# Optimization experiments

Hardware: AMD Instinct MI355X
Metric: run time of the kernel (lower is better)

The kernel has to match this reference:

```python
import jax, jax.numpy as jnp
import numpy as np
import math

B, HR, WR, C = 8, 128, 128, 192
WS, SS = 8, 4
NH, SPH, CHH = 8, 6, 2
DH = C // NH  # 24
AREA = WS * WS
MID = max(C // 4, 8)
NWIN = (HR // WS) * (WR // WS)
LOGMAX = math.log(100.0)

def _rel_pos_index(ws):
    coords = np.stack(np.meshgrid(np.arange(ws), np.arange(ws), indexing='ij')).reshape(2, -1)
    rel = (coords[:, :, None] - coords[:, None, :]).transpose(1, 2, 0).copy()
    rel[:, :, 0] += ws - 1
    rel[:, :, 1] += ws - 1
    rel[:, :, 0] *= 2 * ws - 1
    return rel.sum(-1)  # (AREA, AREA)

def _attn_mask(H, W, ws, ss):
    img = np.zeros((H, W))
    sl = (slice(0, -ws), slice(-ws, -ss), slice(-ss, None))
    cnt = 0
    for hs in sl:
        for wsl in sl:
            img[hs, wsl] = cnt
            cnt += 1
    mw = img.reshape(H // ws, ws, W // ws, ws).transpose(0, 2, 1, 3).reshape(-1, ws * ws)
    am = mw[:, None, :] - mw[:, :, None]
    return np.where(am != 0, -100.0, 0.0).astype(np.float32)

REL_IDX = jnp.asarray(_rel_pos_index(WS))
ATTN_MASK = jnp.asarray(_attn_mask(HR, WR, WS, SS))  # (NWIN, AREA, AREA)

def _norm(v):
    return v / jnp.maximum(jnp.linalg.norm(v, axis=-1, keepdims=True), 1e-12)

def _ln(x, g, b):
    m = x.mean(-1, keepdims=True)
    v = x.var(-1, keepdims=True)
    return (x - m) / jnp.sqrt(v + 1e-5) * g + b

def _bn(x, g, b, m, v):
    return (x - m) / jnp.sqrt(v + 1e-5) * g + b

def _conv3(x, w):  # x: NHWC, w: (O,I,3,3) torch layout
    return jax.lax.conv_general_dilated(x, jnp.transpose(w, (2, 3, 1, 0)), (1, 1), 'SAME', dimension_numbers=('NHWC', 'HWIO', 'NHWC'))

def _forward(x, ln1_g, ln1_b, w_qkv, b_qkv, logit_sp, rpb_table, w_spp, b_spp, logit_ch, w_chp, b_chp, w_sp_proj, w_ch_proj, w_s2c1, w_s2c2, b_s2c2, w_c2s1, w_c2s2, b_c2s2, w_gs1, w_gs2, b_gs2, w_gc1, w_gc2, b_gc2, w_f1, bn1_g, bn1_b, bn1_m, bn1_v, w_f2, bn2_g, bn2_b, bn2_m, bn2_v, w_sg1, w_sg2, b_sg2, ln2_g, ln2_b, w_fc1, b_fc1, w_fc2, b_fc2):
    h = _ln(x, ln1_g, ln1_b)
    img = h.reshape(B, HR, WR, C)
    # qkv conv1x1; per-head channel blocks of 3*DH (faithful to torch view)
    qkv = (img @ w_qkv.T + b_qkv).reshape(B, HR, WR, NH, 3 * DH)
    # ---- spatial shifted-window cosine attention (heads 0:SPH) ----
    sp = jnp.roll(qkv[..., :SPH, :], (-SS, -SS), axis=(1, 2))
    nHw, nWw = HR // WS, WR // WS
    sp = sp.reshape(B, nHw, WS, nWw, WS, SPH, 3 * DH).transpose(0, 1, 3, 5, 2, 4, 6)
    sp = sp.reshape(B * NWIN, SPH, AREA, 3 * DH)
    q, k, v = jnp.split(sp, 3, axis=-1)
    attn = jnp.einsum('bhid,bhjd->bhij', _norm(q), _norm(k))
    attn = attn * jnp.exp(jnp.minimum(logit_sp, LOGMAX)).reshape(1, SPH, 1, 1)
    attn = attn + rpb_table[REL_IDX].transpose(2, 0, 1)[None]
    attn = attn.reshape(B, NWIN, SPH, AREA, AREA) + ATTN_MASK[None, :, None]
    attn = jax.nn.softmax(attn.reshape(B * NWIN, SPH, AREA, AREA), axis=-1)
    o = jnp.einsum('bhij,bhjd->bhid', attn, v)
    o = o.reshape(B, nHw, nWw, SPH, WS, WS, DH).transpose(0, 1, 4, 2, 5, 3, 6).reshape(B, HR, WR, SPH * DH)
    o = o @ w_spp.T + b_spp
    sp_out = jnp.roll(o, (SS, SS), axis=(1, 2)) @ w_sp_proj.T  # (B,H,W,C)
    # ---- channel cosine self-attention (heads SPH:NH) ----
    chq = qkv[..., SPH:, :].reshape(B, HR * WR, CHH, 3 * DH).transpose(0, 2, 3, 1)  # (B,hh,3dh,HW)
    qc, kc, vc = jnp.split(chq, 3, axis=2)
    a = jnp.einsum('bhci,bhdi->bhcd', _norm(qc), _norm(kc))
    a = jax.nn.softmax(a * jnp.exp(jnp.minimum(logit_ch, LOGMAX)).reshape(1, CHH, 1, 1), axis=-1)
    oc = jnp.einsum('bhcd,bhdi->bhci', a, vc).reshape(B, CHH * DH, HR * WR)
    oc = oc.transpose(0, 2, 1).reshape(B, HR, WR, CHH * DH)
    ch_out = (oc @ w_chp.T + b_chp) @ w_ch_proj.T  # (B,H,W,C)
    # ---- CFCA cross gating ----
    def mlp1(t, w1, w2, b2):
        return jax.nn.relu(t @ w1.T) @ w2.T + b2
    sp2ch = mlp1(sp_out, w_s2c1, w_s2c2, b_s2c2) * jax.nn.sigmoid(mlp1(sp_out.mean((1, 2), keepdims=True), w_gs1, w_gs2, b_gs2))
    ch2sp = mlp1(ch_out, w_c2s1, w_c2s2, b_c2s2) * jax.nn.sigmoid(mlp1(ch_out.mean((1, 2), keepdims=True), w_gc1, w_gc2, b_gc2))
    spf = sp_out + ch2sp
    chf = ch_out + sp2ch
    # ---- XFF fusion (BN in eval mode) ----
    f = jnp.concatenate([spf, chf], axis=-1) @ w_f1.T
    f = jax.nn.relu(_bn(f, bn1_g, bn1_b, bn1_m, bn1_v))
    f = jax.nn.relu(_bn(_conv3(f, w_f2), bn2_g, bn2_b, bn2_m, bn2_v))
    g = jax.nn.sigmoid(jax.nn.relu(_conv3(f, w_sg1)) @ w_sg2.T + b_sg2)
    fused = f * g + f
    # ---- transformer block residual + MLP ----
    x = x + fused.reshape(B, HR * WR, C)
    h2 = _ln(x, ln2_g, ln2_b)
    return x + (jax.nn.gelu(h2 @ w_fc1.T + b_fc1, approximate=False) @ w_fc2.T + b_fc2)

def setup_inputs() -> dict:
    keys = iter(jax.random.split(jax.random.key(0), 64))
    def rn(shape, s=0.02):
        return jax.random.normal(next(keys), shape, dtype=jnp.float32) * s
    z = lambda *s: jnp.zeros(s, dtype=jnp.float32)
    o = lambda *s: jnp.ones(s, dtype=jnp.float32)
    return {
        'x': jax.random.normal(next(keys), (B, HR * WR, C), dtype=jnp.float32),
        'ln1_g': o(C), 'ln1_b': z(C),
        'w_qkv': rn((3 * C, C)), 'b_qkv': z(3 * C),
        'logit_sp': jnp.full((SPH,), math.log(10.0), dtype=jnp.float32),
        'rpb_table': rn(((2 * WS - 1) ** 2, SPH)),
        'w_spp': rn((SPH * DH, SPH * DH)), 'b_spp': z(SPH * DH),
        'logit_ch': jnp.full((CHH,), math.log(10.0), dtype=jnp.float32),
        'w_chp': rn((CHH * DH, CHH * DH)), 'b_chp': z(CHH * DH),
        'w_sp_proj': rn((C, SPH * DH)), 'w_ch_proj': rn((C, CHH * DH)),
        'w_s2c1': rn((MID, C)), 'w_s2c2': rn((C, MID)), 'b_s2c2': z(C),
        'w_c2s1': rn((MID, C)), 'w_c2s2': rn((C, MID)), 'b_c2s2': z(C),
        'w_gs1': rn((MID, C)), 'w_gs2': rn((C, MID)), 'b_gs2': z(C),
        'w_gc1': rn((MID, C)), 'w_gc2': rn((C, MID)), 'b_gc2': z(C),
        'w_f1': rn((C, 2 * C)),
        'bn1_g': o(C), 'bn1_b': z(C), 'bn1_m': z(C), 'bn1_v': o(C),
        'w_f2': rn((C, C, 3, 3)),
        'bn2_g': o(C), 'bn2_b': z(C), 'bn2_m': z(C), 'bn2_v': o(C),
        'w_sg1': rn((C // 2, C, 3, 3)), 'w_sg2': rn((1, C // 2)), 'b_sg2': z(1),
        'ln2_g': o(C), 'ln2_b': z(C),
        'w_fc1': rn((4 * C, C)), 'b_fc1': z(4 * C), 'w_fc2': rn((C, 4 * C)), 'b_fc2': z(C),
    }

def reference(x, ln1_g, ln1_b, w_qkv, b_qkv, logit_sp, rpb_table, w_spp, b_spp, logit_ch, w_chp, b_chp, w_sp_proj, w_ch_proj, w_s2c1, w_s2c2, b_s2c2, w_c2s1, w_c2s2, b_c2s2, w_gs1, w_gs2, b_gs2, w_gc1, w_gc2, b_gc2, w_f1, bn1_g, bn1_b, bn1_m, bn1_v, w_f2, bn2_g, bn2_b, bn2_m, bn2_v, w_sg1, w_sg2, b_sg2, ln2_g, ln2_b, w_fc1, b_fc1, w_fc2, b_fc2):
    return _forward(x, ln1_g, ln1_b, w_qkv, b_qkv, logit_sp, rpb_table, w_spp, b_spp, logit_ch, w_chp, b_chp, w_sp_proj, w_ch_proj, w_s2c1, w_s2c2, b_s2c2, w_c2s1, w_c2s2, b_c2s2, w_gs1, w_gs2, b_gs2, w_gc1, w_gc2, b_gc2, w_f1, bn1_g, bn1_b, bn1_m, bn1_v, w_f2, bn2_g, bn2_b, bn2_m, bn2_v, w_sg1, w_sg2, b_sg2, ln2_g, ln2_b, w_fc1, b_fc1, w_fc2, b_fc2)
```

## Files before the change

### kernel.cpp

```cpp
#include <hip/hip_runtime.h>
#include <hip/hip_bf16.h>
#include <cstddef>

typedef __hip_bfloat16 bf16;
typedef unsigned short u16;
typedef unsigned int u32;
typedef short s16x8 __attribute__((ext_vector_type(8)));
typedef float f32x4 __attribute__((ext_vector_type(4)));

#define BATCH 8
#define HR 128
#define WR 128
#define CCH 192
#define HW (HR*WR)
#define MTOK (BATCH*HW)
#define SPH 6
#define SPC 432
#define CHC 144
#define NWIN 256
#define MIDC 48
#define PH 130
#define PHW (PH*PH)
#define LOGMAX 4.6051701859880914f

static const size_t OFF_A0    = 0;
static const size_t OFF_B0    = 113246208;
static const size_t OFF_C0    = 150994944;
static const size_t OFF_SMALL = 188743680;
static const size_t SO_STATS  = 0;
static const size_t SO_PGRAM  = 1048576;
static const size_t SO_PSS    = 1638400;
static const size_t SO_ATTNB  = 1687552;
static const size_t SO_MEANSP = 1724416;
static const size_t SO_MEANCH = 1732608;
static const size_t SO_GATES  = 1740800;
static const size_t SO_GATEC  = 1748992;
static const size_t SO_BCSP   = 1757184;
static const size_t SO_WCCH   = 1758208;
static const size_t SO_BCCH   = 1795072;
static const size_t SO_WFUSE  = 1796096;
static const size_t SO_WCSPB  = 1943552;
static const size_t SO_WQB    = 1998848;
static const size_t SO_WS2C1B = 2220032;
static const size_t SO_WC2S1B = 2238464;
static const size_t SO_WS2C2B = 2256896;
static const size_t SO_WC2S2B = 2275328;
static const size_t SO_WF1B   = 2293760;
static const size_t SO_WF2CB  = 2441216;
static const size_t SO_WSG1CB = 3104768;
static const size_t SO_WFC1B  = 3436544;
static const size_t SO_WFC2B  = 3731456;

__device__ __forceinline__ float b2f(bf16 x) { return __bfloat162float(x); }
__device__ __forceinline__ bf16  f2b(float x){ return __float2bfloat16(x); }
__device__ __forceinline__ u16   f2u(float x){
    bf16 h = __float2bfloat16(x);
    union { bf16 b; u16 u; } c; c.b = h; return c.u;
}
__device__ __forceinline__ float s2f(short s){
    union { u16 u; bf16 b; } c; c.u = (u16)s; return b2f(c.b);
}
__device__ __forceinline__ float u2f(u16 u){
    union { u16 u; bf16 b; } c; c.u = u; return b2f(c.b);
}
__device__ __forceinline__ int xcdswz(int b, int n){
    const int q = n >> 3, r = n & 7, x = b & 7, o = b >> 3;
    return (x < r) ? (x * (q + 1) + o) : (r * (q + 1) + (x - r) * q + o);
}

#define GBM 128
#define GBK 32
#define LDA 40

struct SegRaw { union { uint4 v; struct { float4 lo, hi; } f; } d; };

template<int AMODE, int EPI, int CBF, int BNT, int CPAD, int WPB>
__global__ __launch_bounds__(256)
void gemm_k(const void* __restrict__ A, const u16* __restrict__ W,
            const float* __restrict__ bias, void* __restrict__ Cv,
            int M, int N, int K,
            const float* __restrict__ stats, const float* __restrict__ lng,
            const float* __restrict__ lnb, const void* __restrict__ A2,
            const float* __restrict__ ep0, const float* __restrict__ ep1,
            const float* __restrict__ ep2, const float* __restrict__ ep3)
{
    constexpr int NF = BNT / 32;
    constexpr int NB = (BNT * 4 + 255) / 256;
    constexpr int ATILE = GBM * LDA;
    constexpr int BTILE = BNT * LDA;
    constexpr int BUFSZ = ATILE + BTILE;
    constexpr int CST   = BNT + 8;
    __shared__ u16 smem[2 * BUFSZ];

    const int tid  = threadIdx.x;
    const int lane = tid & 63;
    const int wid  = tid >> 6;
    const int wm   = (wid >> 1) * 64;
    const int wn   = (wid & 1) * (BNT / 2);
    const int m0   = xcdswz(blockIdx.y, gridDim.y) * GBM;
    const int n0   = blockIdx.x * BNT;
    const int row16 = lane & 15;
    const int hi    = lane >> 4;
    const int koff  = hi * 8;

    const int arow[2] = { tid >> 2, (tid + 256) >> 2 };
    const int akk     = (tid & 3) * 8;

    const u16* Wb = W;
    if constexpr (WPB) Wb = W + (size_t)(m0 >> 14) * 9216;

    float meanA[2], rstdA[2];
    if constexpr (AMODE == 1) {
        #pragma unroll
        for (int it = 0; it < 2; ++it) {
            const int m = m0 + arow[it];
            meanA[it] = stats[2*m]; rstdA[it] = stats[2*m+1];
        }
    }

    f32x4 acc[4][NF];
    #pragma unroll
    for (int mf = 0; mf < 4; ++mf)
        #pragma unroll
        for (int nf = 0; nf < NF; ++nf)
            acc[mf][nf] = (f32x4){0.f, 0.f, 0.f, 0.f};

    const int nsteps = (K + GBK - 1) / GBK;

    auto loadA = [&](int step, SegRaw seg[2]) {
        const int k0 = step * GBK;
        #pragma unroll
        for (int it = 0; it < 2; ++it) {
            const int m = m0 + arow[it];
            const int k = k0 + akk;
            SegRaw& s = seg[it];
            if (k >= K) { s.d.v = (uint4){0u,0u,0u,0u}; continue; }
            if constexpr (AMODE == 0) {
                s.d.v = *(const uint4*)((const u16*)A + (size_t)m * K + k);
            } else if constexpr (AMODE == 1) {
                const float* p = (const float*)A + (size_t)m * K + k;
                s.d.f.lo = *(const float4*)p; s.d.f.hi = *(const float4*)(p+4);
            } else if constexpr (AMODE == 2) {
                const u16* src = (k < CCH) ? (const u16*)A  + (size_t)m * CCH + k
                                           : (const u16*)A2 + (size_t)m * CCH + (k - CCH);
                s.d.v = *(const uint4*)src;
            } else if constexpr (AMODE == 3) {
                const int tap = k / CCH, c = k - tap * CCH;
                const int ky = tap / 3, kx = tap - ky * 3;
                const int b = m >> 14, pix = m & 16383;
                const int h = pix >> 7, w = pix & 127;
                s.d.v = *(const uint4*)((const u16*)A +
                        ((size_t)b * PHW + (size_t)(h + ky) * PH + (w + kx)) * CCH + c);
            } else {
                const int col = (k < 24) ? (48 + k) : (96 + k);
                s.d.v = *(const uint4*)((const u16*)A + (size_t)m * CHC + col);
            }
        }
    };
    auto loadB = [&](int step, SegRaw seg[NB]) {
        const int k0 = step * GBK;
        #pragma unroll
        for (int it = 0; it < NB; ++it) {
            const int s = tid + it * 256;
            const int n = n0 + (s >> 2);
            const int k = k0 + (s & 3) * 8;
            seg[it].d.v = (uint4){0u,0u,0u,0u};
            if (s < BNT*4 && k < K && n < N)
                seg[it].d.v = *(const uint4*)(Wb + (size_t)n * K + k);
        }
    };
    auto writeA = [&](int step, SegRaw seg[2], u16* Ab) {
        const int k0 = step * GBK;
        #pragma unroll
        for (int it = 0; it < 2; ++it) {
            if constexpr (AMODE == 1) {
                const int k = k0 + akk;
                union { u16 u[8]; uint4 v; } pk;
                #pragma unroll
                for (int j = 0; j < 8; ++j) {
                    float xx = (j < 4) ? seg[it].d.f.lo[j] : seg[it].d.f.hi[j-4];
                    xx = (xx - meanA[it]) * rstdA[it] * lng[k+j] + lnb[k+j];
                    pk.u[j] = f2u(xx);
                }
                *(uint4*)&Ab[arow[it] * LDA + akk] = pk.v;
            } else {
                *(uint4*)&Ab[arow[it] * LDA + akk] = seg[it].d.v;
            }
        }
    };
    auto writeB = [&](SegRaw seg[NB], u16* Bb) {
        #pragma unroll
        for (int it = 0; it < NB; ++it) {
            const int s = tid + it * 256;
            if (s < BNT*4)
                *(uint4*)&Bb[(s >> 2) * LDA + (s & 3) * 8] = seg[it].d.v;
        }
    };

    SegRaw segA[2], segB[NB];
    loadA(0, segA); loadB(0, segB);
    writeA(0, segA, smem); writeB(segB, smem + ATILE);
    __syncthreads();

    int cur = 0;
    for (int step = 0; step < nsteps; ++step) {
        const bool more = (step + 1 < nsteps);
        if (more) { loadA(step+1, segA); loadB(step+1, segB); }
        u16* Ab = smem + cur * BUFSZ;
        u16* Bb = Ab + ATILE;
        s16x8 af[4], bfr[NF];
        #pragma unroll
        for (int mf = 0; mf < 4; ++mf)
            af[mf] = *(const s16x8*)&Ab[(wm + mf*16 + row16) * LDA + koff];
        #pragma unroll
        for (int nf = 0; nf < NF; ++nf)
            bfr[nf] = *(const s16x8*)&Bb[(wn + nf*16 + row16) * LDA + koff];
        __builtin_amdgcn_s_setprio(1);
        #pragma unroll
        for (int mf = 0; mf < 4; ++mf)
            #pragma unroll
            for (int nf = 0; nf < NF; ++nf)
                acc[mf][nf] = __builtin_amdgcn_mfma_f32_16x16x32_bf16(
                    af[mf], bfr[nf], acc[mf][nf], 0, 0, 0);
        __builtin_amdgcn_s_setprio(0);
        if (more) {
            u16* An = smem + (cur ^ 1) * BUFSZ;
            writeA(step+1, segA, An); writeB(segB, An + ATILE);
        }
        __syncthreads();
        cur ^= 1;
    }

    if constexpr (CBF == 1) {
        #pragma unroll
        for (int mf = 0; mf < 4; ++mf) {
            #pragma unroll
            for (int nf = 0; nf < NF; ++nf) {
                const int n = n0 + wn + nf*16 + row16;
                #pragma unroll
                for (int r = 0; r < 4; ++r) {
                    const int m_loc = wm + mf*16 + hi*4 + r;
                    float v = acc[mf][nf][r];
                    if (n < N) {
                        v += (bias ? bias[n] : 0.f);
                        if constexpr (EPI == 1) {
                            v = fmaxf(v, 0.f);
                        } else if constexpr (EPI == 3) {
                            v = (v - ep2[n]) * rsqrtf(ep3[n] + 1e-5f) * ep0[n] + ep1[n];
                            v = fmaxf(v, 0.f);
                        } else if constexpr (EPI == 4) {
                            const int b = (m0 + m_loc) >> 14;
                            v = v * ep0[b * N + n];
                        } else if constexpr (EPI == 5) {
                            v = 0.5f * v * (1.f + erff(v * 0.70710678118654752f));
                        }
                    }
                    smem[m_loc * CST + (wn + nf*16 + row16)] = f2u(v);
                }
            }
        }
        __syncthreads();
        constexpr int CHUNKS = BNT / 8;
        constexpr int TASKS  = GBM * CHUNKS / 256;
        #pragma unroll
        for (int t2 = 0; t2 < TASKS; ++t2) {
            const int task  = tid + t2 * 256;
            const int rloc  = task / CHUNKS;
            const int chunk = task - rloc * CHUNKS;
            const int m  = m0 + rloc;
            const int nn = n0 + chunk * 8;
            if (nn >= N) continue;
            uint4 val = *(const uint4*)&smem[rloc * CST + chunk * 8];
            if constexpr (EPI == 7) {
                if (nn < SPC) {
                    *(uint4*)((u16*)Cv + (size_t)m * SPC + nn) = val;
                } else {
                    u16* chq = (u16*)ep0;
                    *(uint4*)(chq + (size_t)m * CHC + (nn - SPC)) = val;
                }
                continue;
            }
            size_t outIdx;
            if constexpr (CPAD == 1) {
                const int b = m >> 14, pix = m & 16383;
                const int h = pix >> 7, w = pix & 127;
                outIdx = ((size_t)b * PHW + (size_t)(h+1) * PH + (w+1)) * (size_t)N + nn;
            } else if constexpr (EPI == 2) {
                const int b = m >> 14, pix = m & 16383;
                const int h2 = ((pix >> 7) + 4) & 127;
                const int w2 = ((pix & 127) + 4) & 127;
                outIdx = ((size_t)(b * HW) + h2 * WR + w2) * (size_t)N + nn;
            } else {
                outIdx = (size_t)m * N + nn;
            }
            if constexpr (EPI == 4) {
                union { uint4 v; u16 u[8]; } sv, ov;
                sv.v = val;
                ov.v = *(const uint4*)((const u16*)Cv + outIdx);
                #pragma unroll
                for (int j = 0; j < 8; ++j)
                    sv.u[j] = f2u(u2f(ov.u[j]) + u2f(sv.u[j]));
                *(uint4*)((u16*)Cv + outIdx) = sv.v;
            } else {
                *(uint4*)((u16*)Cv + outIdx) = val;
            }
        }
    } else {
        #pragma unroll
        for (int mf = 0; mf < 4; ++mf) {
            #pragma unroll
            for (int nf = 0; nf < NF; ++nf) {
                const int n = n0 + wn + nf*16 + row16;
                if (n >= N) continue;
                #pragma unroll
                for (int r = 0; r < 4; ++r) {
                    const int m = m0 + wm + mf*16 + hi*4 + r;
                    float v = acc[mf][nf][r] + (bias ? bias[n] : 0.f);
                    const size_t outIdx = (size_t)m * N + n;
                    if constexpr (EPI == 6) v = ep0[outIdx] + v;
                    ((float*)Cv)[outIdx] = v;
                }
            }
        }
    }
}

__global__ __launch_bounds__(256)
void wprep_lin_k(const float* __restrict__ in, bf16* __restrict__ outb, int n)
{
    const int i = blockIdx.x * 256 + threadIdx.x;
    if (i < n) outb[i] = f2b(in[i]);
}

__global__ __launch_bounds__(256)
void wprep_conv_k(const float* __restrict__ in, bf16* __restrict__ outb, int total)
{
    const int i = blockIdx.x * 256 + threadIdx.x;
    if (i >= total) return;
    const int n = i / 1728, r = i - n * 1728;
    const int tap = r / CCH, c = r - tap * CCH;
    outb[i] = f2b(in[((size_t)n * CCH + c) * 9 + tap]);
}

__global__ __launch_bounds__(256)
void zb_k(bf16* __restrict__ buf)
{
    const int i = blockIdx.x * 256 + threadIdx.x;
    if (i >= 8 * 516 * 24) return;
    const int chunk = i % 24;
    const int p = (i / 24) % 516;
    const int b = i / (24 * 516);
    int h, w;
    if (p < 130)      { h = 0;   w = p; }
    else if (p < 260) { h = 129; w = p - 130; }
    else { const int q = p - 260; h = 1 + (q >> 1); w = (q & 1) ? 129 : 0; }
    *(uint4*)((u16*)buf + ((size_t)b * PHW + (size_t)h * PH + w) * CCH + chunk * 8)
        = (uint4){0u,0u,0u,0u};
}

__global__ __launch_bounds__(256)
void zerof_k(float* __restrict__ p, int n)
{
    const int i = blockIdx.x * 256 + threadIdx.x;
    if (i < n) p[i] = 0.f;
}

__global__ __launch_bounds__(256)
void ln_stats_k(const float* __restrict__ x, float* __restrict__ stats)
{
    const int tok = blockIdx.x * 4 + (threadIdx.x >> 6);
    const int lane = threadIdx.x & 63;
    const float* r = x + (size_t)tok * CCH;
    float s = 0.f, sq = 0.f;
    for (int c = lane; c < CCH; c += 64) { float v = r[c]; s += v; sq += v*v; }
    for (int m = 1; m < 64; m <<= 1) { s += __shfl_xor(s, m); sq += __shfl_xor(sq, m); }
    if (lane == 0) {
        const float mean = s / (float)CCH;
        const float var = sq / (float)CCH - mean * mean;
        stats[(size_t)tok*2]   = mean;
        stats[(size_t)tok*2+1] = rsqrtf(var + 1e-5f);
    }
}

__global__ __launch_bounds__(384)
void sp_attn_k(const bf16* __restrict__ spqkv, const float* __restrict__ rpb,
               const float* __restrict__ logit_sp, bf16* __restrict__ osp)
{
    const int b    = blockIdx.x >> 8;
    const int win  = blockIdx.x & 255;
    const int wh = win >> 4, ww = win & 15;
    const int head = threadIdx.x >> 6;
    const int lane = threadIdx.x & 63;
    const int row16 = lane & 15;
    const int hi   = lane >> 4;
    const int koff = hi * 8;

    __shared__ float rpbS[1350];
    __shared__ u16 vT[SPH][32][72];

    for (int i = threadIdx.x; i < 1350; i += 384) rpbS[i] = rpb[i];

    const u16* base = (const u16*)spqkv + (size_t)b * HW * SPC;

    s16x8 qf[4], kf[4];
    const int wcol = (ww*8 + (row16 & 7) + 4) & 127;
    #pragma unroll
    for (int t = 0; t < 4; ++t) {
        const int pos = t*16 + row16;
        const int h = (wh*8 + (pos >> 3) + 4) & 127;
        const u16* rowp = base + ((size_t)(h * WR + wcol)) * SPC + head * 72;
        if (koff < 24) {
            qf[t] = *(const s16x8*)(rowp + koff);
            kf[t] = *(const s16x8*)(rowp + 24 + koff);
        } else {
            qf[t] = (s16x8){0,0,0,0,0,0,0,0};
            kf[t] = (s16x8){0,0,0,0,0,0,0,0};
        }
    }

    {
        const int h = (wh*8 + (lane >> 3) + 4) & 127;
        const int w = (ww*8 + (lane & 7) + 4) & 127;
        const u16* vrow = base + ((size_t)(h * WR + w)) * SPC + head * 72 + 48;
        union { uint4 v; u16 u[8]; } seg[3];
        seg[0].v = *(const uint4*)(vrow);
        seg[1].v = *(const uint4*)(vrow + 8);
        seg[2].v = *(const uint4*)(vrow + 16);
        #pragma unroll
        for (int d = 0; d < 24; ++d) vT[head][d][lane] = seg[d>>3].u[d&7];
        #pragma unroll
        for (int d = 24; d < 32; ++d) vT[head][d][lane] = 0;
    }
    __syncthreads();

    float rq[4], rk[4];
    #pragma unroll
    for (int t = 0; t < 4; ++t) {
        float sq = 0.f, sk = 0.f;
        #pragma unroll
        for (int e = 0; e < 8; ++e) {
            const float a = s2f(qf[t][e]); sq += a*a;
            const float c = s2f(kf[t][e]); sk += c*c;
        }
        sq += __shfl_xor(sq, 16); sq += __shfl_xor(sq, 32);
        sk += __shfl_xor(sk, 16); sk += __shfl_xor(sk, 32);
        rq[t] = 1.f / fmaxf(sqrtf(sq), 1e-12f);
        rk[t] = 1.f / fmaxf(sqrtf(sk), 1e-12f);
    }
    const float scale_h = __expf(fminf(logit_sp[head], LOGMAX));

    f32x4 acc[4][4];
    #pragma unroll
    for (int mfk = 0; mfk < 4; ++mfk)
        #pragma unroll
        for (int nfq = 0; nfq < 4; ++nfq)
            acc[mfk][nfq] = (f32x4){0.f,0.f,0.f,0.f};
    #pragma unroll
    for (int mfk = 0; mfk < 4; ++mfk)
        #pragma unroll
        for (int nfq = 0; nfq < 4; ++nfq)
            acc[mfk][nfq] = __builtin_amdgcn_mfma_f32_16x16x32_bf16(
                kf[mfk], qf[nfq], acc[mfk][nfq], 0, 0, 0);

    f32x4 rkj[4];
    #pragma unroll
    for (int mfk = 0; mfk < 4; ++mfk)
        #pragma unroll
        for (int r = 0; r < 4; ++r)
            rkj[mfk][r] = __shfl(rk[mfk], hi*4 + r);

    int ip3[4], iw7[4], labi[4];
    #pragma unroll
    for (int t = 0; t < 4; ++t) {
        const int pos = t*16 + row16;
        ip3[t] = pos >> 3; iw7[t] = pos & 7;
        const int hh = wh*8 + ip3[t], w0 = ww*8 + iw7[t];
        const int rh = hh < 120 ? 0 : (hh < 124 ? 1 : 2);
        const int rw = w0 < 120 ? 0 : (w0 < 124 ? 1 : 2);
        labi[t] = rh*3 + rw;
    }

    #pragma unroll
    for (int mfk = 0; mfk < 4; ++mfk) {
        #pragma unroll
        for (int r = 0; r < 4; ++r) {
            const int j = hi*4 + r + 16*mfk;
            const int jp3 = j >> 3, jw7 = j & 7;
            const int hh = wh*8 + jp3, w0 = ww*8 + jw7;
            const int rh = hh < 120 ? 0 : (hh < 124 ? 1 : 2);
            const int rw = w0 < 120 ? 0 : (w0 < 124 ? 1 : 2);
            const int labj = rh*3 + rw;
            const float rkv = rkj[mfk][r];
            #pragma unroll
            for (int nfq = 0; nfq < 4; ++nfq) {
                float s = acc[mfk][nfq][r] * rq[nfq] * rkv * scale_h;
                s += rpbS[((ip3[nfq]-jp3+7)*15 + (iw7[nfq]-jw7+7))*SPH + head];
                if (labi[nfq] != labj) s -= 100.f;
                acc[mfk][nfq][r] = s;
            }
        }
    }

    float inv[4];
    #pragma unroll
    for (int nfq = 0; nfq < 4; ++nfq) {
        float m = -1e30f;
        #pragma unroll
        for (int mfk = 0; mfk < 4; ++mfk)
            #pragma unroll
            for (int r = 0; r < 4; ++r)
                m = fmaxf(m, acc[mfk][nfq][r]);
        m = fmaxf(m, __shfl_xor(m, 16));
        m = fmaxf(m, __shfl_xor(m, 32));
        float s = 0.f;
        #pragma unroll
        for (int mfk = 0; mfk < 4; ++mfk)
            #pragma unroll
            for (int r = 0; r < 4; ++r) {
                const float p = __expf(acc[mfk][nfq][r] - m);
                acc[mfk][nfq][r] = p;
                s += p;
            }
        s += __shfl_xor(s, 16);
        s += __shfl_xor(s, 32);
        inv[nfq] = 1.f / s;
    }

    u32 pk01[4][4], pk23[4][4];
    #pragma unroll
    for (int mfk = 0; mfk < 4; ++mfk)
        #pragma unroll
        for (int nfq = 0; nfq < 4; ++nfq) {
            pk01[mfk][nfq] = (u32)f2u(acc[mfk][nfq][0] * inv[nfq])
                           | ((u32)f2u(acc[mfk][nfq][1] * inv[nfq]) << 16);
            pk23[mfk][nfq] = (u32)f2u(acc[mfk][nfq][2] * inv[nfq])
                           | ((u32)f2u(acc[mfk][nfq][3] * inv[nfq]) << 16);
        }

    s16x8 vf[2][2];
    #pragma unroll
    for (int nf = 0; nf < 2; ++nf)
        #pragma unroll
        for (int ks = 0; ks < 2; ++ks)
            vf[nf][ks] = *(const s16x8*)&vT[head][row16 + 16*nf][32*ks + koff];

    f32x4 accO[4][2];
    #pragma unroll
    for (int MF = 0; MF < 4; ++MF)
        #pragma unroll
        for (int nf = 0; nf < 2; ++nf)
            accO[MF][nf] = (f32x4){0.f,0.f,0.f,0.f};

    const int g0 = 2*(hi & 1);
    const int src0 = g0*16 + row16, src1 = src0 + 16;
    const bool selhi = (hi >> 1) != 0;
    #pragma unroll
    for (int ks = 0; ks < 2; ++ks) {
        #pragma unroll
        for (int MF = 0; MF < 4; ++MF) {
            const u32 e01a = __shfl(pk01[2*ks][MF],   src0);
            const u32 e01b = __shfl(pk01[2*ks+1][MF], src0);
            const u32 e23a = __shfl(pk23[2*ks][MF],   src0);
            const u32 e23b = __shfl(pk23[2*ks+1][MF], src0);
            const u32 e45a = __shfl(pk01[2*ks][MF],   src1);
            const u32 e45b = __shfl(pk01[2*ks+1][MF], src1);
            const u32 e67a = __shfl(pk23[2*ks][MF],   src1);
            const u32 e67b = __shfl(pk23[2*ks+1][MF], src1);
            union { u32 w[4]; s16x8 v; } af;
            af.w[0] = selhi ? e01b : e01a;
            af.w[1] = selhi ? e23b : e23a;
            af.w[2] = selhi ? e45b : e45a;
            af.w[3] = selhi ? e67b : e67a;
            accO[MF][0] = __builtin_amdgcn_mfma_f32_16x16x32_bf16(
                af.v, vf[0][ks], accO[MF][0], 0, 0, 0);
            accO[MF][1] = __builtin_amdgcn_mfma_f32_16x16x32_bf16(
                af.v, vf[1][ks], accO[MF][1], 0, 0, 0);
        }
    }

    #pragma unroll
    for (int MF = 0; MF < 4; ++MF) {
        #pragma unroll
        for (int nf = 0; nf < 2; ++nf) {
            const int d = row16 + 16*nf;
            if (d >= 24) continue;
            #pragma unroll
            for (int r = 0; r < 4; ++r) {
                const int qrow = hi*4 + r + 16*MF;
                const int h = wh*8 + (qrow >> 3);
                const int w = ww*8 + (qrow & 7);
                osp[((size_t)b*HW + h*WR + w)*144 + head*24 + d] = f2b(accO[MF][nf][r]);
            }
        }
    }
}

__global__ __launch_bounds__(256)
void ch_part_k(const bf16* __restrict__ chqkv, float* __restrict__ pgram,
               float* __restrict__ pss)
{
    const int ci = blockIdx.x, head = blockIdx.y, b = blockIdx.z;
    const int tid = threadIdx.x;
    __shared__ u16 tile[256][48];
    float g[3] = {0.f, 0.f, 0.f};
    float ss = 0.f;
    const u16* src = (const u16*)chqkv + (size_t)b * HW * CHC + head * 72;
    const int rbase = ci * 1024;

    for (int t0 = 0; t0 < 1024; t0 += 256) {
        __syncthreads();
        for (int idx = tid; idx < 256*6; idx += 256) {
            const int row = idx / 6, seg = idx - (idx/6)*6;
            *(uint4*)&tile[row][seg*8] =
                *(const uint4*)(src + (size_t)(rbase + t0 + row) * CHC + seg*8);
        }
        __syncthreads();
        #pragma unroll
        for (int i = 0; i < 3; ++i) {
            const int e = tid + i*256;
            if (e < 576) {
                const int c = e / 24, d = e - (e/24)*24;
                float s = 0.f;
                for (int r = 0; r < 256; ++r)
                    s += b2f(*(const bf16*)&tile[r][c]) * b2f(*(const bf16*)&tile[r][24+d]);
                g[i] += s;
            }
        }
        if (tid < 48) {
            float s = 0.f;
            for (int r = 0; r < 256; ++r) { const float v = b2f(*(const bf16*)&tile[r][tid]); s += v*v; }
            ss += s;
        }
    }
    float* pg = pgram + ((size_t)(b*2+head)*16 + ci) * 576;
    #pragma unroll
    for (int i = 0; i < 3; ++i) { const int e = tid + i*256; if (e < 576) pg[e] = g[i]; }
    if (tid < 48) pss[((size_t)(b*2+head)*16 + ci) * 48 + tid] = ss;
}

__global__ __launch_bounds__(256)
void ch_soft_k(const float* __restrict__ pgram, const float* __restrict__ pss,
               const float* __restrict__ logit_ch, float* __restrict__ attn)
{
    const int head = blockIdx.x, b = blockIdx.y;
    const int tid = threadIdx.x;
    __shared__ float gs[576], rn[48];
    for (int e = tid; e < 576; e += 256) {
        float s = 0.f;
        const float* pg = pgram + (size_t)(b*2+head)*16*576 + e;
        for (int c = 0; c < 16; ++c) s += pg[c*576];
        gs[e] = s;
    }
    if (tid < 48) {
        float s = 0.f;
        const float* ps = pss + (size_t)(b*2+head)*16*48 + tid;
        for (int c = 0; c < 16; ++c) s += ps[c*48];
        rn[tid] = 1.f / fmaxf(sqrtf(s), 1e-12f);
    }
    __syncthreads();
    if (tid < 24) {
        const float scale = expf(fminf(logit_ch[head], LOGMAX));
        float vals[24], mx = -1e30f;
        #pragma unroll
        for (int d = 0; d < 24; ++d) {
            vals[d] = gs[tid*24+d] * rn[tid] * rn[24+d] * scale;
            mx = fmaxf(mx, vals[d]);
        }
        float sum = 0.f;
        #pragma unroll
        for (int d = 0; d < 24; ++d) { vals[d] = expf(vals[d]-mx); sum += vals[d]; }
        const float inv = 1.f / sum;
        float* o = attn + ((size_t)(b*2+head)*24 + tid)*24;
        #pragma unroll
        for (int d = 0; d < 24; ++d) o[d] = vals[d]*inv;
    }
}

__global__ __launch_bounds__(192)
void fuse_chw_k(const float* __restrict__ Wc, const float* __restrict__ attn,
                bf16* __restrict__ Wf)
{
    const int b = blockIdx.x;
    const int n = threadIdx.x;
    __shared__ float As_[2][24][24];
    for (int e = n; e < 1152; e += 192) {
        const int h = e / 576, r = e - h*576;
        As_[h][r/24][r%24] = attn[(size_t)b*1152 + e];
    }
    __syncthreads();
    const float* wr = Wc + n*48;
    bf16* o = Wf + ((size_t)b*192 + n) * 48;
    for (int h = 0; h < 2; ++h)
        for (int d = 0; d < 24; ++d) {
            float s = 0.f;
            #pragma unroll
            for (int cc = 0; cc < 24; ++cc) s += wr[h*24+cc] * As_[h][cc][d];
            o[h*24+d] = f2b(s);
        }
}

__global__ void combine_sp_k(const float* __restrict__ w_sp_proj, const float* __restrict__ w_spp,
                             const float* __restrict__ b_spp, bf16* __restrict__ Wc, float* __restrict__ bc)
{
    const int n = blockIdx.x;
    for (int i = threadIdx.x; i < 144; i += blockDim.x) {
        float s = 0.f;
        for (int j = 0; j < 144; ++j) s += w_sp_proj[n*144 + j] * w_spp[j*144 + i];
        Wc[n*144 + i] = f2b(s);
    }
    if (threadIdx.x == 0) {
        float s = 0.f;
        for (int j = 0; j < 144; ++j) s += w_sp_proj[n*144 + j] * b_spp[j];
        bc[n] = s;
    }
}

__global__ void combine_ch_k(const float* __restrict__ w_ch_proj, const float* __restrict__ w_chp,
                             const float* __restrict__ b_chp, float* __restrict__ Wc, float* __restrict__ bc)
{
    const int n = blockIdx.x;
    for (int c = threadIdx.x; c < 48; c += blockDim.x) {
        float s = 0.f;
        for (int j = 0; j < 48; ++j) s += w_ch_proj[n*48 + j] * w_chp[j*48 + c];
        Wc[n*48 + c] = s;
    }
    if (threadIdx.x == 0) {
        float s = 0.f;
        for (int j = 0; j < 48; ++j) s += w_ch_proj[n*48 + j] * b_chp[j];
        bc[n] = s;
    }
}

__global__ __launch_bounds__(256)
void mean2_k(const bf16* __restrict__ src, float* __restrict__ dst)
{
    const int b = blockIdx.y;
    const int r0 = blockIdx.x * 256;
    const int t = threadIdx.x;
    const int chunk = t & 31;
    const int rg = t >> 5;
    float acc[8] = {0.f,0.f,0.f,0.f,0.f,0.f,0.f,0.f};
    if (chunk < 24) {
        for (int r = rg; r < 256; r += 8) {
            const u16* p = (const u16*)src + ((size_t)(b*HW) + r0 + r) * CCH + chunk*8;
            union { uint4 v; u16 u[8]; } s; s.v = *(const uint4*)p;
            #pragma unroll
            for (int j = 0; j < 8; ++j) acc[j] += u2f(s.u[j]);
        }
    }
    __shared__ float red[8][24][8];
    if (chunk < 24) {
        #pragma unroll
        for (int j = 0; j < 8; ++j) red[rg][chunk][j] = acc[j];
    }
    __syncthreads();
    if (t < 192) {
        const int ch = t >> 3, j = t & 7;
        float s = 0.f;
        #pragma unroll
        for (int g = 0; g < 8; ++g) s += red[g][ch][j];
        atomicAdd(&dst[b*CCH + ch*8 + j], s);
    }
}

__global__ __launch_bounds__(192)
void gates_k(const float* __restrict__ sumv, const float* __restrict__ w1,
             const float* __restrict__ w2, const float* __restrict__ b2,
             float* __restrict__ gate)
{
    const int b = blockIdx.x;
    __shared__ float mv[192], hid[48];
    const int t = threadIdx.x;
    mv[t] = sumv[b*CCH + t] * (1.f / (float)HW);
    __syncthreads();
    if (t < 48) {
        float s = 0.f;
        for (int c = 0; c < 192; ++c) s += w1[t*192 + c] * mv[c];
        hid[t] = fmaxf(s, 0.f);
    }
    __syncthreads();
    float s = b2[t];
    for (int j = 0; j < 48; ++j) s += hid[j] * w2[t*48 + j];
    gate[b*CCH + t] = 1.f / (1.f + expf(-s));
}

__global__ __launch_bounds__(256)
void fuse_k(const float* __restrict__ x, const bf16* __restrict__ f2pad,
            const bf16* __restrict__ gpre, const float* __restrict__ w_sg2,
            const float* __restrict__ b_sg2, float* __restrict__ out)
{
    const int pix = blockIdx.x * 4 + (threadIdx.x >> 6);
    const int lane = threadIdx.x & 63;
    const bf16* gp = gpre + (size_t)pix * 96;
    float s = fmaxf(b2f(gp[lane]), 0.f) * w_sg2[lane];
    if (lane < 32) s += fmaxf(b2f(gp[lane + 64]), 0.f) * w_sg2[lane + 64];
    for (int m = 1; m < 64; m <<= 1) s += __shfl_xor(s, m);
    const float g1 = 1.f + 1.f / (1.f + expf(-(s + b_sg2[0])));
    const int b = pix >> 14, p = pix & 16383;
    const int h = p >> 7, w = p & 127;
    const bf16* fr = f2pad + ((size_t)b * PHW + (size_t)(h+1) * PH + (w+1)) * CCH;
    const float* xr = x + (size_t)pix * CCH;
    float* orow = out + (size_t)pix * CCH;
    for (int c = lane; c < CCH; c += 64) orow[c] = xr[c] + b2f(fr[c]) * g1;
}

extern "C" void kernel_launch(void* const* d_in, const int* in_sizes, int n_in,
                              void* d_out, int out_size, void* d_ws, size_t ws_size,
                              hipStream_t stream)
{
    const float* x        = (const float*)d_in[0];
    const float* ln1_g    = (const float*)d_in[1];
    const float* ln1_b    = (const float*)d_in[2];
    const float* w_qkv    = (const float*)d_in[3];
    const float* b_qkv    = (const float*)d_in[4];
    const float* logit_sp = (const float*)d_in[5];
    const float* rpb      = (const float*)d_in[6];
    const float* w_spp    = (const float*)d_in[7];
    const float* b_spp    = (const float*)d_in[8];
    const float* logit_ch = (const float*)d_in[9];
    const float* w_chp    = (const float*)d_in[10];
    const float* b_chp    = (const float*)d_in[11];
    const float* w_sp_proj= (const float*)d_in[12];
    const float* w_ch_proj= (const float*)d_in[13];
    const float* w_s2c1   = (const float*)d_in[14];
    const float* w_s2c2   = (const float*)d_in[15];
    const float* b_s2c2   = (const float*)d_in[16];
    const float* w_c2s1   = (const float*)d_in[17];
    const float* w_c2s2   = (const float*)d_in[18];
    const float* b_c2s2   = (const float*)d_in[19];
    const float* w_gs1    = (const float*)d_in[20];
    const float* w_gs2    = (const float*)d_in[21];
    const float* b_gs2    = (const float*)d_in[22];
    const float* w_gc1    = (const float*)d_in[23];
    const float* w_gc2    = (const float*)d_in[24];
    const float* b_gc2    = (const float*)d_in[25];
    const float* w_f1     = (const float*)d_in[26];
    const float* bn1_g    = (const float*)d_in[27];
    const float* bn1_b    = (const float*)d_in[28];
    const float* bn1_m    = (const float*)d_in[29];
    const float* bn1_v    = (const float*)d_in[30];
    const float* w_f2     = (const float*)d_in[31];
    const float* bn2_g    = (const float*)d_in[32];
    const float* bn2_b    = (const float*)d_in[33];
    const float* bn2_m    = (const float*)d_in[34];
    const float* bn2_v    = (const float*)d_in[35];
    const float* w_sg1    = (const float*)d_in[36];
    const float* w_sg2    = (const float*)d_in[37];
    const float* b_sg2    = (const float*)d_in[38];
    const float* ln2_g    = (const float*)d_in[39];
    const float* ln2_b    = (const float*)d_in[40];
    const float* w_fc1    = (const float*)d_in[41];
    const float* b_fc1    = (const float*)d_in[42];
    const float* w_fc2    = (const float*)d_in[43];
    const float* b_fc2    = (const float*)d_in[44];

    char* wsb = (char*)d_ws;
    char* sm  = wsb + OFF_SMALL;
    float* out = (float*)d_out;

    bf16*  spqkv  = (bf16*)(wsb + OFF_A0);
    bf16*  sp_out = (bf16*)(wsb + OFF_A0);
    bf16*  ch_out = (bf16*)(wsb + OFF_A0 + 50331648);
    bf16*  f2pad  = (bf16*)(wsb + OFF_A0);
    bf16*  gpre   = (bf16*)(wsb + OFF_A0 + 51916800);
    bf16*  chqkv  = (bf16*)(wsb + OFF_B0);
    bf16*  hid_s  = (bf16*)(wsb + OFF_B0);
    bf16*  hid_c  = (bf16*)(wsb + OFF_B0 + 12582912);
    bf16*  fpad   = (bf16*)(wsb + OFF_B0);
    bf16*  hidden = (bf16*)(wsb + OFF_A0);
    bf16*  osp    = (bf16*)(wsb + OFF_C0);

    float* stats  = (float*)(sm + SO_STATS);
    float* pgram  = (float*)(sm + SO_PGRAM);
    float* pss    = (float*)(sm + SO_PSS);
    float* attn_b = (float*)(sm + SO_ATTNB);
    float* mean_sp= (float*)(sm + SO_MEANSP);
    float* mean_ch= (float*)(sm + SO_MEANCH);
    float* gate_s = (float*)(sm + SO_GATES);
    float* gate_c = (float*)(sm + SO_GATEC);
    float* bc_sp  = (float*)(sm + SO_BCSP);
    float* Wc_ch  = (float*)(sm + SO_WCCH);
    float* bc_ch  = (float*)(sm + SO_BCCH);
    bf16*  Wfuse  = (bf16*)(sm + SO_WFUSE);
    bf16*  Wc_spB = (bf16*)(sm + SO_WCSPB);
    u16*   wqB    = (u16*)(sm + SO_WQB);
    u16*   ws2c1B = (u16*)(sm + SO_WS2C1B);
    u16*   wc2s1B = (u16*)(sm + SO_WC2S1B);
    u16*   ws2c2B = (u16*)(sm + SO_WS2C2B);
    u16*   wc2s2B = (u16*)(sm + SO_WC2S2B);
    u16*   wf1B   = (u16*)(sm + SO_WF1B);
    u16*   wf2cB  = (u16*)(sm + SO_WF2CB);
    u16*   wsg1cB = (u16*)(sm + SO_WSG1CB);
    u16*   wfc1B  = (u16*)(sm + SO_WFC1B);
    u16*   wfc2B  = (u16*)(sm + SO_WFC2B);

    const dim3 blk(256);

    wprep_lin_k<<<(110592+255)/256, blk, 0, stream>>>(w_qkv,  (bf16*)wqB,    110592);
    wprep_lin_k<<<(9216+255)/256,   blk, 0, stream>>>(w_s2c1, (bf16*)ws2c1B, 9216);
    wprep_lin_k<<<(9216+255)/256,   blk, 0, stream>>>(w_c2s1, (bf16*)wc2s1B, 9216);
    wprep_lin_k<<<(9216+255)/256,   blk, 0, stream>>>(w_s2c2, (bf16*)ws2c2B, 9216);
    wprep_lin_k<<<(9216+255)/256,   blk, 0, stream>>>(w_c2s2, (bf16*)wc2s2B, 9216);
    wprep_lin_k<<<(73728+255)/256,  blk, 0, stream>>>(w_f1,   (bf16*)wf1B,   73728);
    wprep_lin_k<<<(147456+255)/256, blk, 0, stream>>>(w_fc1,  (bf16*)wfc1B,  147456);
    wprep_lin_k<<<(147456+255)/256, blk, 0, stream>>>(w_fc2,  (bf16*)wfc2B,  147456);
    wprep_conv_k<<<(331776+255)/256, blk, 0, stream>>>(w_f2,  (bf16*)wf2cB,  331776);
    wprep_conv_k<<<(165888+255)/256, blk, 0, stream>>>(w_sg1, (bf16*)wsg1cB, 165888);
    combine_sp_k<<<192, 128, 0, stream>>>(w_sp_proj, w_spp, b_spp, Wc_spB, bc_sp);
    combine_ch_k<<<192, 64, 0, stream>>>(w_ch_proj, w_chp, b_chp, Wc_ch, bc_ch);
    zerof_k<<<6, blk, 0, stream>>>(mean_sp, 1536);
    zerof_k<<<6, blk, 0, stream>>>(mean_ch, 1536);

    ln_stats_k<<<MTOK/4, blk, 0, stream>>>(x, stats);
    gemm_k<1,7,1,192,0,0><<<dim3(3, MTOK/GBM), blk, 0, stream>>>(
        x, wqB, b_qkv, spqkv, MTOK, 576, CCH,
        stats, ln1_g, ln1_b, nullptr,
        (const float*)chqkv, nullptr, nullptr, nullptr);

    sp_attn_k<<<dim3(BATCH*NWIN), dim3(384), 0, stream>>>(spqkv, rpb, logit_sp, osp);
    gemm_k<0,2,1,192,0,0><<<dim3(1, MTOK/GBM), blk, 0, stream>>>(
        osp, (const u16*)Wc_spB, bc_sp, sp_out, MTOK, CCH, 144,
        nullptr, nullptr, nullptr, nullptr,
        nullptr, nullptr, nullptr, nullptr);

    ch_part_k<<<dim3(16, 2, BATCH), blk, 0, stream>>>(chqkv, pgram, pss);
    ch_soft_k<<<dim3(2, BATCH), blk, 0, stream>>>(pgram, pss, logit_ch, attn_b);
    fuse_chw_k<<<BATCH, 192, 0, stream>>>(Wc_ch, attn_b, Wfuse);
    gemm_k<4,0,1,192,0,1><<<dim3(1, MTOK/GBM), blk, 0, stream>>>(
        chqkv, (const u16*)Wfuse, bc_ch, ch_out, MTOK, CCH, 48,
        nullptr, nullptr, nullptr, nullptr,
        nullptr, nullptr, nullptr, nullptr);

    mean2_k<<<dim3(HW/256, BATCH), blk, 0, stream>>>(sp_out, mean_sp);
    mean2_k<<<dim3(HW/256, BATCH), blk, 0, stream>>>(ch_out, mean_ch);
    gates_k<<<BATCH, 192, 0, stream>>>(mean_sp, w_gs1, w_gs2, b_gs2, gate_s);
    gates_k<<<BATCH, 192, 0, stream>>>(mean_ch, w_gc1, w_gc2, b_gc2, gate_c);

    gemm_k<0,1,1,96,0,0><<<dim3(1, MTOK/GBM), blk, 0, stream>>>(
        sp_out, ws2c1B, nullptr, hid_s, MTOK, MIDC, CCH,
        nullptr, nullptr, nullptr, nullptr, nullptr, nullptr, nullptr, nullptr);
    gemm_k<0,1,1,96,0,0><<<dim3(1, MTOK/GBM), blk, 0, stream>>>(
        ch_out, wc2s1B, nullptr, hid_c, MTOK, MIDC, CCH,
        nullptr, nullptr, nullptr, nullptr, nullptr, nullptr, nullptr, nullptr);
    gemm_k<0,4,1,192,0,0><<<dim3(1, MTOK/GBM), blk, 0, stream>>>(
        hid_s, ws2c2B, b_s2c2, ch_out, MTOK, CCH, MIDC,
        nullptr, nullptr, nullptr, nullptr, gate_s, nullptr, nullptr, nullptr);
    gemm_k<0,4,1,192,0,0><<<dim3(1, MTOK/GBM), blk, 0, stream>>>(
        hid_c, wc2s2B, b_c2s2, sp_out, MTOK, CCH, MIDC,
        nullptr, nullptr, nullptr, nullptr, gate_c, nullptr, nullptr, nullptr);

    zb_k<<<(8*516*24+255)/256, blk, 0, stream>>>(fpad);
    gemm_k<2,3,1,192,1,0><<<dim3(1, MTOK/GBM), blk, 0, stream>>>(
        sp_out, wf1B, nullptr, fpad, MTOK, CCH, 2*CCH,
        nullptr, nullptr, nullptr, ch_out, bn1_g, bn1_b, bn1_m, bn1_v);

    zb_k<<<(8*516*24+255)/256, blk, 0, stream>>>(f2pad);
    gemm_k<3,3,1,192,1,0><<<dim3(1, MTOK/GBM), blk, 0, stream>>>(
        fpad, wf2cB, nullptr, f2pad, MTOK, CCH, 9*CCH,
        nullptr, nullptr, nullptr, nullptr, bn2_g, bn2_b, bn2_m, bn2_v);

    gemm_k<3,0,1,96,0,0><<<dim3(1, MTOK/GBM), blk, 0, stream>>>(
        f2pad, wsg1cB, nullptr, gpre, MTOK, 96, 9*CCH,
        nullptr, nullptr, nullptr, nullptr, nullptr, nullptr, nullptr, nullptr);

    fuse_k<<<MTOK/4, blk, 0, stream>>>(x, f2pad, gpre, w_sg2, b_sg2, out);

    ln_stats_k<<<MTOK/4, blk, 0, stream>>>(out, stats);
    const int CHM = MTOK / 2;
    for (int c0 = 0; c0 < MTOK; c0 += CHM) {
        gemm_k<1,5,1,192,0,0><<<dim3(4, CHM/GBM), blk, 0, stream>>>(
            out + (size_t)c0*CCH, wfc1B, b_fc1, hidden, CHM, 4*CCH, CCH,
            stats + (size_t)c0*2, ln2_g, ln2_b, nullptr,
            nullptr, nullptr, nullptr, nullptr);
        gemm_k<0,6,0,192,0,0><<<dim3(1, CHM/GBM), blk, 0, stream>>>(
            hidden, wfc2B, b_fc2, out + (size_t)c0*CCH, CHM, CCH, 4*CCH,
            nullptr, nullptr, nullptr, nullptr, out + (size_t)c0*CCH,
            nullptr, nullptr, nullptr);
    }
}
```

Measured before the change: 1.341 ms.

## Load GEMM B fragments directly from global into registers, halve epilogue LDS

The weight (B) operand no longer goes through shared memory. Each lane now loads its MFMA B fragment straight from global memory into registers and double-buffers it in registers, so shared memory holds only the A tiles. The bf16 epilogue staging is split into two 64-row halves, which shrinks the LDS footprint and may raise occupancy. The cost is redundant global reads of weights, since both M-wave pairs fetch the same B rows and rely on cache, plus less coalesced B loads and an extra barrier in the epilogue.

```diff
diff --git a/kernel.cpp b/kernel.cpp
--- a/kernel.cpp
+++ b/kernel.cpp
@@ -85,12 +85,11 @@
             const float* __restrict__ ep2, const float* __restrict__ ep3)
 {
     constexpr int NF = BNT / 32;
-    constexpr int NB = (BNT * 4 + 255) / 256;
     constexpr int ATILE = GBM * LDA;
-    constexpr int BTILE = BNT * LDA;
-    constexpr int BUFSZ = ATILE + BTILE;
     constexpr int CST   = BNT + 8;
-    __shared__ u16 smem[2 * BUFSZ];
+    constexpr int CSTG  = 64 * CST;
+    constexpr int SMEMSZ = (2 * ATILE > CSTG) ? 2 * ATILE : CSTG;
+    __shared__ u16 smem[SMEMSZ];
 
     const int tid  = threadIdx.x;
     const int lane = tid & 63;
@@ -108,6 +107,14 @@
 
     const u16* Wb = W;
     if constexpr (WPB) Wb = W + (size_t)(m0 >> 14) * 9216;
+
+    const u16* bp[NF];
+    #pragma unroll
+    for (int nf = 0; nf < NF; ++nf) {
+        int n = n0 + wn + nf*16 + row16;
+        if (n >= N) n = N - 1;
+        bp[nf] = Wb + (size_t)n * K;
+    }
 
     float meanA[2], rstdA[2];
     if constexpr (AMODE == 1) {
@@ -157,17 +164,13 @@
             }
         }
     };
-    auto loadB = [&](int step, SegRaw seg[NB]) {
+    auto loadBfrag = [&](int step, s16x8 dst[NF]) {
         const int k0 = step * GBK;
-        #pragma unroll
-        for (int it = 0; it < NB; ++it) {
-            const int s = tid + it * 256;
-            const int n = n0 + (s >> 2);
-            const int k = k0 + (s & 3) * 8;
-            seg[it].d.v = (uint4){0u,0u,0u,0u};
-            if (s < BNT*4 && k < K && n < N)
-                seg[it].d.v = *(const uint4*)(Wb + (size_t)n * K + k);
-        }
+        const bool kin = (k0 + koff + 8 <= K);
+        #pragma unroll
+        for (int nf = 0; nf < NF; ++nf)
+            dst[nf] = kin ? *(const s16x8*)(bp[nf] + k0 + koff)
+                          : (s16x8){0,0,0,0,0,0,0,0};
     };
     auto writeA = [&](int step, SegRaw seg[2], u16* Ab) {
         const int k0 = step * GBK;
@@ -188,121 +191,116 @@
             }
         }
     };
-    auto writeB = [&](SegRaw seg[NB], u16* Bb) {
-        #pragma unroll
-        for (int it = 0; it < NB; ++it) {
-            const int s = tid + it * 256;
-            if (s < BNT*4)
-                *(uint4*)&Bb[(s >> 2) * LDA + (s & 3) * 8] = seg[it].d.v;
-        }
-    };
-
-    SegRaw segA[2], segB[NB];
-    loadA(0, segA); loadB(0, segB);
-    writeA(0, segA, smem); writeB(segB, smem + ATILE);
+
+    SegRaw segA[2];
+    s16x8 bcur[NF], bnxt[NF];
+    loadA(0, segA);
+    loadBfrag(0, bcur);
+    writeA(0, segA, smem);
     __syncthreads();
 
     int cur = 0;
     for (int step = 0; step < nsteps; ++step) {
         const bool more = (step + 1 < nsteps);
-        if (more) { loadA(step+1, segA); loadB(step+1, segB); }
-        u16* Ab = smem + cur * BUFSZ;
-        u16* Bb = Ab + ATILE;
-        s16x8 af[4], bfr[NF];
+        if (more) { loadA(step+1, segA); loadBfrag(step+1, bnxt); }
+        u16* Ab = smem + cur * ATILE;
+        s16x8 af[4];
         #pragma unroll
         for (int mf = 0; mf < 4; ++mf)
             af[mf] = *(const s16x8*)&Ab[(wm + mf*16 + row16) * LDA + koff];
-        #pragma unroll
-        for (int nf = 0; nf < NF; ++nf)
-            bfr[nf] = *(const s16x8*)&Bb[(wn + nf*16 + row16) * LDA + koff];
         __builtin_amdgcn_s_setprio(1);
         #pragma unroll
         for (int mf = 0; mf < 4; ++mf)
             #pragma unroll
             for (int nf = 0; nf < NF; ++nf)
                 acc[mf][nf] = __builtin_amdgcn_mfma_f32_16x16x32_bf16(
-                    af[mf], bfr[nf], acc[mf][nf], 0, 0, 0);
+                    af[mf], bcur[nf], acc[mf][nf], 0, 0, 0);
         __builtin_amdgcn_s_setprio(0);
         if (more) {
-            u16* An = smem + (cur ^ 1) * BUFSZ;
-            writeA(step+1, segA, An); writeB(segB, An + ATILE);
+            writeA(step+1, segA, smem + (cur ^ 1) * ATILE);
+            #pragma unroll
+            for (int nf = 0; nf < NF; ++nf) bcur[nf] = bnxt[nf];
         }
         __syncthreads();
         cur ^= 1;
     }
 
     if constexpr (CBF == 1) {
-        #pragma unroll
-        for (int mf = 0; mf < 4; ++mf) {
-            #pragma unroll
-            for (int nf = 0; nf < NF; ++nf) {
-                const int n = n0 + wn + nf*16 + row16;
+        constexpr int CHUNKS = BNT / 8;
+        #pragma unroll
+        for (int hh = 0; hh < 2; ++hh) {
+            __syncthreads();
+            if ((wid >> 1) == hh) {
                 #pragma unroll
-                for (int r = 0; r < 4; ++r) {
-                    const int m_loc = wm + mf*16 + hi*4 + r;
-                    float v = acc[mf][nf][r];
-                    if (n < N) {
-                        v += (bias ? bias[n] : 0.f);
-                        if constexpr (EPI == 1) {
-                            v = fmaxf(v, 0.f);
-                        } else if constexpr (EPI == 3) {
-                            v = (v - ep2[n]) * rsqrtf(ep3[n] + 1e-5f) * ep0[n] + ep1[n];
-                            v = fmaxf(v, 0.f);
-                        } else if constexpr (EPI == 4) {
-                            const int b = (m0 + m_loc) >> 14;
-                            v = v * ep0[b * N + n];
-                        } else if constexpr (EPI == 5) {
-                            v = 0.5f * v * (1.f + erff(v * 0.70710678118654752f));
+                for (int mf = 0; mf < 4; ++mf) {
+                    #pragma unroll
+                    for (int nf = 0; nf < NF; ++nf) {
+                        const int n = n0 + wn + nf*16 + row16;
+                        #pragma unroll
+                        for (int r = 0; r < 4; ++r) {
+                            const int mloc = mf*16 + hi*4 + r;
+                            float v = acc[mf][nf][r];
+                            if (n < N) {
+                                v += (bias ? bias[n] : 0.f);
+                                if constexpr (EPI == 1) {
+                                    v = fmaxf(v, 0.f);
+                                } else if constexpr (EPI == 3) {
+                                    v = (v - ep2[n]) * rsqrtf(ep3[n] + 1e-5f) * ep0[n] + ep1[n];
+                                    v = fmaxf(v, 0.f);
+                                } else if constexpr (EPI == 4) {
+                                    const int b = (m0 + hh*64 + mloc) >> 14;
+                                    v = v * ep0[b * N + n];
+                                } else if constexpr (EPI == 5) {
+                                    v = 0.5f * v * (1.f + erff(v * 0.70710678118654752f));
+                                }
+                            }
+                            smem[mloc * CST + (wn + nf*16 + row16)] = f2u(v);
                         }
                     }
-                    smem[m_loc * CST + (wn + nf*16 + row16)] = f2u(v);
                 }
             }
-        }
-        __syncthreads();
-        constexpr int CHUNKS = BNT / 8;
-        constexpr int TASKS  = GBM * CHUNKS / 256;
-        #pragma unroll
-        for (int t2 = 0; t2 < TASKS; ++t2) {
-            const int task  = tid + t2 * 256;
-            const int rloc  = task / CHUNKS;
-            const int chunk = task - rloc * CHUNKS;
-            const int m  = m0 + rloc;
-            const int nn = n0 + chunk * 8;
-            if (nn >= N) continue;
-            uint4 val = *(const uint4*)&smem[rloc * CST + chunk * 8];
-            if constexpr (EPI == 7) {
-                if (nn < SPC) {
-                    *(uint4*)((u16*)Cv + (size_t)m * SPC + nn) = val;
+            __syncthreads();
+            const int TOT = 64 * CHUNKS;
+            for (int task = tid; task < TOT; task += 256) {
+                const int rloc  = task / CHUNKS;
+                const int chunk = task - rloc * CHUNKS;
+                const int m  = m0 + hh*64 + rloc;
+                const int nn = n0 + chunk * 8;
+                if (nn >= N) continue;
+                uint4 val = *(const uint4*)&smem[rloc * CST + chunk * 8];
+                if constexpr (EPI == 7) {
+                    if (nn < SPC) {
+                        *(uint4*)((u16*)Cv + (size_t)m * SPC + nn) = val;
+                    } else {
+                        u16* chq = (u16*)ep0;
+                        *(uint4*)(chq + (size_t)m * CHC + (nn - SPC)) = val;
+                    }
+                    continue;
+                }
+                size_t outIdx;
+                if constexpr (CPAD == 1) {
+                    const int b = m >> 14, pix = m & 16383;
+                    const int h = pix >> 7, w = pix & 127;
+                    outIdx = ((size_t)b * PHW + (size_t)(h+1) * PH + (w+1)) * (size_t)N + nn;
+                } else if constexpr (EPI == 2) {
+                    const int b = m >> 14, pix = m & 16383;
+                    const int h2 = ((pix >> 7) + 4) & 127;
+                    const int w2 = ((pix & 127) + 4) & 127;
+                    outIdx = ((size_t)(b * HW) + h2 * WR + w2) * (size_t)N + nn;
                 } else {
-                    u16* chq = (u16*)ep0;
-                    *(uint4*)(chq + (size_t)m * CHC + (nn - SPC)) = val;
+                    outIdx = (size_t)m * N + nn;
                 }
-                continue;
-            }
-            size_t outIdx;
-            if constexpr (CPAD == 1) {
-                const int b = m >> 14, pix = m & 16383;
-                const int h = pix >> 7, w = pix & 127;
-                outIdx = ((size_t)b * PHW + (size_t)(h+1) * PH + (w+1)) * (size_t)N + nn;
-            } else if constexpr (EPI == 2) {
-                const int b = m >> 14, pix = m & 16383;
-                const int h2 = ((pix >> 7) + 4) & 127;
-                const int w2 = ((pix & 127) + 4) & 127;
-                outIdx = ((size_t)(b * HW) + h2 * WR + w2) * (size_t)N + nn;
-            } else {
-                outIdx = (size_t)m * N + nn;
-            }
-            if constexpr (EPI == 4) {
-                union { uint4 v; u16 u[8]; } sv, ov;
-                sv.v = val;
-                ov.v = *(const uint4*)((const u16*)Cv + outIdx);
-                #pragma unroll
-                for (int j = 0; j < 8; ++j)
-                    sv.u[j] = f2u(u2f(ov.u[j]) + u2f(sv.u[j]));
-                *(uint4*)((u16*)Cv + outIdx) = sv.v;
-            } else {
-                *(uint4*)((u16*)Cv + outIdx) = val;
+                if constexpr (EPI == 4) {
+                    union { uint4 v; u16 u[8]; } sv, ov;
+                    sv.v = val;
+                    ov.v = *(const uint4*)((const u16*)Cv + outIdx);
+                    #pragma unroll
+                    for (int j = 0; j < 8; ++j)
+                        sv.u[j] = f2u(u2f(ov.u[j]) + u2f(sv.u[j]));
+                    *(uint4*)((u16*)Cv + outIdx) = sv.v;
+                } else {
+                    *(uint4*)((u16*)Cv + outIdx) = val;
+                }
             }
         }
     } else {
```

Result: slower. 2.921 ms (+117.8%).
